# Kernel optimization log

Measured on AMD Instinct MI355X. Metric: run time of the kernel, lower is better.

The kernel has to match this reference:

```python
import jax, jax.numpy as jnp
import numpy as np

A_MAX = 7  # 2**A_bits - 1 with A_bits=3
W_HI = 7   # torch.randint(0, 2**W_bits - 1) -> values in [0, 6]


def _conv_valid(x, w):
    # x: [N,C,H,W] float32, w: [O,I,kh,kw] float32; stride 1, no padding
    return jax.lax.conv_general_dilated(
        x, w, window_strides=(1, 1), padding='VALID',
        dimension_numbers=('NCHW', 'OIHW', 'NCHW'))


def setup_inputs() -> dict:
    key = jax.random.key(0)
    k_x, k_w = jax.random.split(key)
    x = jax.random.randint(k_x, (16, 64, 112, 112), 0, 8, dtype=jnp.int32)
    # 3-bit weights of the original 7x7 conv, values 0..6
    W7 = jax.random.randint(k_w, (128, 64, 7, 7), 0, W_HI).astype(jnp.float32)
    w1 = W7[:, :, :, 0:3]
    w2 = W7[:, :, :, 2:5]
    w2 = w2.at[:, :, :, 0].set(0.0)
    w2 = w2.at[:, :, :, 2].set(0.0)
    w3 = W7[:, :, :, 4:7]
    return {"x": x, "w1": w1, "w2": w2, "w3": w3}


def reference(x, w1, w2, w3):
    # 3-bit activation quantization: clip int input to [0, 7]
    xc = jnp.clip(x, 0, A_MAX).astype(jnp.float32)
    out1 = _conv_valid(xc[:, :, :, :-2], w1)   # [N,O,H-6,W-4]
    out2 = _conv_valid(xc, w2)                 # [N,O,H-6,W-2]
    out3 = _conv_valid(xc[:, :, :, 2:], w3)    # [N,O,H-6,W-4]
    # combine slices -> equivalent to valid 7x7 conv: [N,O,H-6,W-6]
    return out1[:, :, :, :-2] + out2[:, :, :, 2:-2] + out3[:, :, :, 2:]
```

## Files before the change

kernel.cpp:

```cpp
#include <hip/hip_runtime.h>
#include <cstdint>

typedef __attribute__((ext_vector_type(4))) int i32x4;

#define XROWS  22
#define ROWB   2048
#define WSLICE 8192
#define WB_BYTES 409600
#define XT_BYTES ((size_t)16 * 112 * 128 * 64)
#define NTILES 1568
#define GRID_MAIN 1536

__device__ __forceinline__ void g2lds16(const void* g, void* l) {
  __builtin_amdgcn_global_load_lds(
      (const __attribute__((address_space(1))) unsigned int*)g,
      (__attribute__((address_space(3))) unsigned int*)l, 16, 0, 0);
}

__global__ void prep_w(const float* __restrict__ w1,
                       const float* __restrict__ w2,
                       const float* __restrict__ w3,
                       signed char* __restrict__ wb) {
  int t = blockIdx.x * 256 + threadIdx.x;
  int lo = t & 15;
  int co = (t >> 4) & 127;
  int g  = (t >> 11) & 3;
  int s  = t >> 13;
  if (s >= 49) return;
  int kh = s / 7, kw = s % 7;
  int ci = g * 16 + lo;
  int base = ((co * 64 + ci) * 7 + kh) * 3;
  float v;
  if (kw < 3)       v = w1[base + kw];
  else if (kw == 3) v = w2[base + 1];
  else              v = w3[base + kw - 4];
  wb[t] = (signed char)(int)v;
}

__global__ void prep_xw(const int* __restrict__ x,
                        const float* __restrict__ w1,
                        const float* __restrict__ w2,
                        const float* __restrict__ w3,
                        signed char* __restrict__ xt,
                        signed char* __restrict__ wb) {
  __shared__ unsigned char T[64 * 68];
  const int tid = threadIdx.x;
  const int wt = blockIdx.x * 64, h = blockIdx.y, n = blockIdx.z;
  const int fid = (blockIdx.z * 112 + blockIdx.y) * 2 + blockIdx.x;

  if (fid < 1568) {
    int t = fid * 256 + tid;
    int lo = t & 15;
    int co = (t >> 4) & 127;
    int g  = (t >> 11) & 3;
    int s  = t >> 13;
    int kh = s / 7, kw = s % 7;
    int ci = g * 16 + lo;
    int base = ((co * 64 + ci) * 7 + kh) * 3;
    float v;
    if (kw < 3)       v = w1[base + kw];
    else if (kw == 3) v = w2[base + 1];
    else              v = w3[base + kw - 4];
    wb[t] = (signed char)(int)v;
  }

  {
    const int wr = tid & 63;
    const int cb = (tid >> 6) * 16;
    int ws = wt + wr; ws = ws < 112 ? ws : 111;
    const int* xp = x + (((size_t)n * 64 + cb) * 112 + h) * 112 + ws;
    #pragma unroll
    for (int g4 = 0; g4 < 4; ++g4) {
      uint32_t v = 0;
      #pragma unroll
      for (int j = 0; j < 4; ++j) {
        int a = xp[(g4 * 4 + j) * 12544];
        a = a < 0 ? 0 : (a > 7 ? 7 : a);
        v |= (uint32_t)a << (8 * j);
      }
      *(uint32_t*)&T[wr * 68 + cb + g4 * 4] = v;
    }
  }
  __syncthreads();
  {
    const int wo = tid >> 2, q = tid & 3;
    const int key = ((wt + wo) >> 1) & 3;
    const int sg = (q ^ key) << 4;
    int4 v;
    v.x = *(const int*)&T[wo * 68 + sg + 0];
    v.y = *(const int*)&T[wo * 68 + sg + 4];
    v.z = *(const int*)&T[wo * 68 + sg + 8];
    v.w = *(const int*)&T[wo * 68 + sg + 12];
    *(int4*)&xt[(((size_t)n * 112 + h) * 128 + wt + wo) * 64 + q * 16] = v;
  }
}

#define MFMA(acc, a, b) acc = __builtin_amdgcn_mfma_i32_16x16x64_i8(a, b, acc, 0, 0, 0)

__global__ __launch_bounds__(256, 3)
void conv7s(const signed char* __restrict__ xt,
            const signed char* __restrict__ wb,
            float* __restrict__ out) {
  __shared__ __align__(16) unsigned char Xs[XROWS * ROWB];

  const int tid  = threadIdx.x;
  const int lane = tid & 63;
  const int wid  = tid >> 6;
  const int lrow = lane & 15;
  const int lkg  = lane >> 4;

  const int L  = blockIdx.x;
  const int Lp = (L & 7) * 192 + (L >> 3);
  const int npass = (L < 32) ? 2 : 1;

  for (int pass = 0; pass < npass; ++pass) {
    const int t = (pass == 0) ? Lp : (GRID_MAIN + L);
    const int coh = t & 1;
    const int r2  = t >> 1;
    const int bx  = r2 % 7;
    const int t7  = r2 / 7;
    const int by  = t7 % 7;
    const int n   = t7 / 7;
    const int ho_base = by * 16;
    const int wo_base = bx * 16;

    const signed char* aB = wb + lkg * 2048 + (coh * 64 + wid * 16 + lrow) * 16;

    i32x4 Aa = *(const i32x4*)aB;
    i32x4 Ab;

    if (pass) __syncthreads();

    for (int r = wid; r < XROWS; r += 4) {
      int h = ho_base + r; h = h < 112 ? h : 111;
      const signed char* src = xt + (((size_t)n * 112 + h) * 128 + wo_base) * 64;
      g2lds16(src + lane * 16, &Xs[r * ROWB]);
      g2lds16(src + 1024 + lane * 16, &Xs[r * ROWB + 1024]);
    }
    asm volatile("s_waitcnt vmcnt(0)" ::: "memory");
    __syncthreads();

    i32x4 acc[16];
    #pragma unroll
    for (int j = 0; j < 16; ++j) acc[j] = (i32x4){0, 0, 0, 0};

    for (int kw = 0; kw < 7; ++kw) {
      const int w_l  = lrow + kw;
      const int bcol = w_l * 64 + ((lkg ^ ((w_l >> 1) & 3)) << 4);
      i32x4 B[16];
      #pragma unroll
      for (int b = 0; b < 16; ++b)
        B[b] = *(const i32x4*)&Xs[b * ROWB + bcol];

      #pragma unroll
      for (int kh = 0; kh < 7; ++kh) {
        const signed char* apn =
            aB + (size_t)(kh < 6 ? (kh + 1) * 7 + kw : (kw < 6 ? kw + 1 : 0)) * WSLICE;
        __builtin_amdgcn_s_setprio(1);
        if ((kh & 1) == 0) {
          Ab = *(const i32x4*)apn;
          #pragma unroll
          for (int j = 0; j < 16; ++j)
            MFMA(acc[j], Aa, B[(kh + j) & 15]);
        } else {
          Aa = *(const i32x4*)apn;
          #pragma unroll
          for (int j = 0; j < 16; ++j)
            MFMA(acc[j], Ab, B[(kh + j) & 15]);
        }
        __builtin_amdgcn_s_setprio(0);
        if (kh < 6)
          B[kh] = *(const i32x4*)&Xs[(kh + 16) * ROWB + bcol];
      }
      Aa = Ab;
    }

    const int wo = wo_base + lrow;
    if (wo < 106) {
      const int co = coh * 64 + wid * 16 + lkg * 4;
      #pragma unroll
      for (int j = 0; j < 16; ++j) {
        const int ho = ho_base + j;
        if (ho < 106) {
          float* op = out + (((size_t)n * 128 + co) * 106 + ho) * 106 + wo;
          #pragma unroll
          for (int jj = 0; jj < 4; ++jj)
            op[(size_t)jj * 11236] = (float)acc[j][jj];
        }
      }
    }
  }
}

__global__ __launch_bounds__(256, 3)
void conv7f(const int* __restrict__ x,
            const signed char* __restrict__ wb, float* __restrict__ out) {
  __shared__ __align__(16) unsigned char Xs[XROWS * ROWB];

  const int tid  = threadIdx.x;
  const int lane = tid & 63;
  const int wid  = tid >> 6;
  const int lrow = lane & 15;
  const int lkg  = lane >> 4;

  const int L  = blockIdx.x;
  const int Lp = (L & 7) * 196 + (L >> 3);
  const int coh = Lp & 1;
  const int r2  = Lp >> 1;
  const int bx  = r2 % 7;
  const int t7  = r2 / 7;
  const int by  = t7 % 7;
  const int n   = t7 / 7;
  const int ho_base = by * 16;
  const int wo_base = bx * 16;

  const signed char* aB = wb + lkg * 2048 + coh * 1024 + lrow * 16;
  i32x4 A[4];
  #pragma unroll
  for (int m = 0; m < 4; ++m) A[m] = *(const i32x4*)(aB + m * 256);

  {
    const int w_a  = tid & 15,       cg_a  = tid >> 4;
    const int w_b2 = 16 + (tid & 7), cg_b2 = tid >> 3;
    const bool doB = (tid < 128) && ((tid & 7) < 6);
    const int keyA = ((w_a >> 1) & 3) << 2;
    const int keyB = ((w_b2 >> 1) & 3) << 2;
    for (int r = 0; r < XROWS; ++r) {
      int h = ho_base + r; h = h < 112 ? h : 111;
      const int* xr = x + (size_t)n * 64 * 12544 + h * 112;
      {
        int wc = wo_base + w_a; wc = wc < 112 ? wc : 111;
        uint32_t v = 0;
        #pragma unroll
        for (int j = 0; j < 4; ++j) {
          int a = xr[(cg_a * 4 + j) * 12544 + wc];
          a = a < 0 ? 0 : (a > 7 ? 7 : a);
          v |= (uint32_t)a << (8 * j);
        }
        *(uint32_t*)&Xs[r * ROWB + w_a * 64 + ((cg_a ^ keyA) << 2)] = v;
      }
      if (doB) {
        int wc = wo_base + w_b2; wc = wc < 112 ? wc : 111;
        uint32_t v = 0;
        #pragma unroll
        for (int j = 0; j < 4; ++j) {
          int a = xr[(cg_b2 * 4 + j) * 12544 + wc];
          a = a < 0 ? 0 : (a > 7 ? 7 : a);
          v |= (uint32_t)a << (8 * j);
        }
        *(uint32_t*)&Xs[r * ROWB + w_b2 * 64 + ((cg_b2 ^ keyB) << 2)] = v;
      }
    }
  }
  __syncthreads();

  i32x4 acc[4][4];
  #pragma unroll
  for (int m = 0; m < 4; ++m)
    #pragma unroll
    for (int b = 0; b < 4; ++b)
      acc[m][b] = (i32x4){0, 0, 0, 0};

  const int rowB = wid * 4;

  for (int kw = 0; kw < 7; ++kw) {
    const int w_l  = lrow + kw;
    const int bcol = w_l * 64 + ((lkg ^ ((w_l >> 1) & 3)) << 4);
    i32x4 B[8];
    #pragma unroll
    for (int b = 0; b < 4; ++b)
      B[b] = *(const i32x4*)&Xs[(rowB + b) * ROWB + bcol];
    #pragma unroll
    for (int kh = 0; kh < 7; ++kh) {
      if (kh < 6)
        B[(kh + 4) & 7] = *(const i32x4*)&Xs[(rowB + kh + 4) * ROWB + bcol];
      const signed char* apn = aB + (size_t)(kh < 6 ? (kh + 1) * 7 + kw : kw + 1) * WSLICE;
      #pragma unroll
      for (int m = 0; m < 4; ++m) {
        #pragma unroll
        for (int b = 0; b < 4; ++b)
          MFMA(acc[m][b], A[m], B[(kh + b) & 7]);
        A[m] = *(const i32x4*)(apn + m * 256);
      }
    }
  }

  const int wo = wo_base + lrow;
  if (wo < 106) {
    #pragma unroll
    for (int m = 0; m < 4; ++m) {
      const int co = coh * 64 + m * 16 + lkg * 4;
      #pragma unroll
      for (int b = 0; b < 4; ++b) {
        const int ho = ho_base + rowB + b;
        if (ho < 106) {
          float* op = out + (((size_t)n * 128 + co) * 106 + ho) * 106 + wo;
          #pragma unroll
          for (int j = 0; j < 4; ++j)
            op[(size_t)j * 11236] = (float)acc[m][b][j];
        }
      }
    }
  }
}

extern "C" void kernel_launch(void* const* d_in, const int* in_sizes, int n_in,
                              void* d_out, int out_size, void* d_ws, size_t ws_size,
                              hipStream_t stream) {
  const int*   x  = (const int*)d_in[0];
  const float* w1 = (const float*)d_in[1];
  const float* w2 = (const float*)d_in[2];
  const float* w3 = (const float*)d_in[3];
  float* outp = (float*)d_out;
  signed char* wbp = (signed char*)d_ws;
  signed char* xtp = wbp + WB_BYTES;

  if (ws_size >= WB_BYTES + XT_BYTES) {
    prep_xw<<<dim3(2, 112, 16), dim3(256), 0, stream>>>(x, w1, w2, w3, xtp, wbp);
    conv7s<<<dim3(GRID_MAIN), dim3(256), 0, stream>>>(xtp, wbp, outp);
  } else {
    prep_w<<<dim3(1568), dim3(256), 0, stream>>>(w1, w2, w3, wbp);
    conv7f<<<dim3(1568), dim3(256), 0, stream>>>(x, wbp, outp);
  }
}
```

Before: 70.95 us.

## Switch main conv kernel from 16x16x64 to 32x32x32 int8 MFMA tiles

Rewrites the main convolution kernel to use 32x32x32 int8 MFMA instructions instead of 16x16x64. Each wave now covers 32 output channels by two interleaved output rows, and K is split into two 32-channel halves. The weight prep layout is reordered to match the new K split. The goal is fewer MFMA issues and fewer LDS B-fragment loads per output element. The cost is a new register and accumulator layout, larger 16-wide accumulators, and a more scattered store pattern.

```diff
diff --git a/kernel.cpp b/kernel.cpp
--- a/kernel.cpp
+++ b/kernel.cpp
@@ -2,13 +2,12 @@
 #include <cstdint>
 
 typedef __attribute__((ext_vector_type(4))) int i32x4;
+typedef __attribute__((ext_vector_type(16))) int i32x16;
 
 #define XROWS  22
 #define ROWB   2048
-#define WSLICE 8192
 #define WB_BYTES 409600
 #define XT_BYTES ((size_t)16 * 112 * 128 * 64)
-#define NTILES 1568
 #define GRID_MAIN 1536
 
 __device__ __forceinline__ void g2lds16(const void* g, void* l) {
@@ -50,12 +49,13 @@
 
   if (fid < 1568) {
     int t = fid * 256 + tid;
-    int lo = t & 15;
+    int b  = t & 15;
     int co = (t >> 4) & 127;
-    int g  = (t >> 11) & 3;
+    int hk = (t >> 11) & 1;
+    int k2 = (t >> 12) & 1;
     int s  = t >> 13;
     int kh = s / 7, kw = s % 7;
-    int ci = g * 16 + lo;
+    int ci = k2 * 32 + hk * 16 + b;
     int base = ((co * 64 + ci) * 7 + kh) * 3;
     float v;
     if (kw < 3)       v = w1[base + kw];
@@ -95,10 +95,11 @@
   }
 }
 
-#define MFMA(acc, a, b) acc = __builtin_amdgcn_mfma_i32_16x16x64_i8(a, b, acc, 0, 0, 0)
+#define MFMA16(acc, a, b) acc = __builtin_amdgcn_mfma_i32_16x16x64_i8(a, b, acc, 0, 0, 0)
+#define MFMA32(acc, a, b) acc = __builtin_amdgcn_mfma_i32_32x32x32_i8(a, b, acc, 0, 0, 0)
 
 __global__ __launch_bounds__(256, 3)
-void conv7s(const signed char* __restrict__ xt,
+void conv32(const signed char* __restrict__ xt,
             const signed char* __restrict__ wb,
             float* __restrict__ out) {
   __shared__ __align__(16) unsigned char Xs[XROWS * ROWB];
@@ -106,8 +107,12 @@
   const int tid  = threadIdx.x;
   const int lane = tid & 63;
   const int wid  = tid >> 6;
-  const int lrow = lane & 15;
-  const int lkg  = lane >> 4;
+  const int l15  = lane & 15;
+  const int l4   = (lane >> 4) & 1;
+  const int l5   = lane >> 5;
+  const int cohalf = wid >> 1;
+  const int sph    = wid & 1;
+  const int spbase = sph * 8;
 
   const int L  = blockIdx.x;
   const int Lp = (L & 7) * 192 + (L >> 3);
@@ -124,10 +129,8 @@
     const int ho_base = by * 16;
     const int wo_base = bx * 16;
 
-    const signed char* aB = wb + lkg * 2048 + (coh * 64 + wid * 16 + lrow) * 16;
-
-    i32x4 Aa = *(const i32x4*)aB;
-    i32x4 Ab;
+    const signed char* aB =
+        wb + l5 * 2048 + (coh * 64 + cohalf * 32 + (lane & 31)) * 16;
 
     if (pass) __syncthreads();
 
@@ -140,52 +143,71 @@
     asm volatile("s_waitcnt vmcnt(0)" ::: "memory");
     __syncthreads();
 
-    i32x4 acc[16];
-    #pragma unroll
-    for (int j = 0; j < 16; ++j) acc[j] = (i32x4){0, 0, 0, 0};
+    i32x16 acc[4];
+    #pragma unroll
+    for (int tt = 0; tt < 4; ++tt)
+      acc[tt] = (i32x16){0,0,0,0, 0,0,0,0, 0,0,0,0, 0,0,0,0};
+
+    i32x4 Aa = *(const i32x4*)aB;
+    i32x4 Ab;
 
     for (int kw = 0; kw < 7; ++kw) {
-      const int w_l  = lrow + kw;
-      const int bcol = w_l * 64 + ((lkg ^ ((w_l >> 1) & 3)) << 4);
-      i32x4 B[16];
-      #pragma unroll
-      for (int b = 0; b < 16; ++b)
-        B[b] = *(const i32x4*)&Xs[b * ROWB + bcol];
-
-      #pragma unroll
-      for (int kh = 0; kh < 7; ++kh) {
-        const signed char* apn =
-            aB + (size_t)(kh < 6 ? (kh + 1) * 7 + kw : (kw < 6 ? kw + 1 : 0)) * WSLICE;
-        __builtin_amdgcn_s_setprio(1);
-        if ((kh & 1) == 0) {
-          Ab = *(const i32x4*)apn;
+      const int w_l = l15 + kw;
+      const int key = (w_l >> 1) & 3;
+      const int rbase = (spbase + l4) * ROWB + w_l * 64;
+      const int cb0 = rbase + (((0 + l5) ^ key) << 4);
+      const int cb1 = rbase + (((2 + l5) ^ key) << 4);
+      #pragma unroll
+      for (int k2 = 0; k2 < 2; ++k2) {
+        const int cb = k2 ? cb1 : cb0;
+        i32x4 Be[4], Bo[4];
+        #pragma unroll
+        for (int p = 0; p < 4; ++p) {
+          Be[p] = *(const i32x4*)&Xs[cb + (2 * p) * ROWB];
+          Bo[p] = *(const i32x4*)&Xs[cb + (2 * p + 1) * ROWB];
+        }
+        #pragma unroll
+        for (int kh = 0; kh < 7; ++kh) {
+          const int nkh = (kh < 6) ? kh + 1 : 0;
+          const int nk2 = (kh < 6) ? k2 : (k2 ^ 1);
+          const int nkw = (kh < 6) ? kw : (k2 == 0 ? kw : (kw < 6 ? kw + 1 : 0));
+          const signed char* apn = aB + (size_t)((nkh * 7 + nkw) * 2 + nk2) * 4096;
+          __builtin_amdgcn_s_setprio(1);
+          if ((kh & 1) == 0) {
+            Ab = *(const i32x4*)apn;
+            #pragma unroll
+            for (int tt = 0; tt < 4; ++tt)
+              MFMA32(acc[tt], Aa, Be[(tt + (kh >> 1)) & 3]);
+          } else {
+            Aa = *(const i32x4*)apn;
+            #pragma unroll
+            for (int tt = 0; tt < 4; ++tt)
+              MFMA32(acc[tt], Ab, Bo[(tt + (kh >> 1)) & 3]);
+          }
+          __builtin_amdgcn_s_setprio(0);
+          if (kh == 0)      Be[0] = *(const i32x4*)&Xs[cb +  8 * ROWB];
+          else if (kh == 1) Bo[0] = *(const i32x4*)&Xs[cb +  9 * ROWB];
+          else if (kh == 2) Be[1] = *(const i32x4*)&Xs[cb + 10 * ROWB];
+          else if (kh == 3) Bo[1] = *(const i32x4*)&Xs[cb + 11 * ROWB];
+          else if (kh == 4) Be[2] = *(const i32x4*)&Xs[cb + 12 * ROWB];
+        }
+        Aa = Ab;
+      }
+    }
+
+    const int wo = wo_base + l15;
+    if (wo < 106) {
+      #pragma unroll
+      for (int tt = 0; tt < 4; ++tt) {
+        const int ho = ho_base + spbase + 2 * tt + l4;
+        if (ho < 106) {
+          float* op = out +
+              (((size_t)n * 128 + coh * 64 + cohalf * 32) * 106 + ho) * 106 + wo;
           #pragma unroll
-          for (int j = 0; j < 16; ++j)
-            MFMA(acc[j], Aa, B[(kh + j) & 15]);
-        } else {
-          Aa = *(const i32x4*)apn;
-          #pragma unroll
-          for (int j = 0; j < 16; ++j)
-            MFMA(acc[j], Ab, B[(kh + j) & 15]);
-        }
-        __builtin_amdgcn_s_setprio(0);
-        if (kh < 6)
-          B[kh] = *(const i32x4*)&Xs[(kh + 16) * ROWB + bcol];
-      }
-      Aa = Ab;
-    }
-
-    const int wo = wo_base + lrow;
-    if (wo < 106) {
-      const int co = coh * 64 + wid * 16 + lkg * 4;
-      #pragma unroll
-      for (int j = 0; j < 16; ++j) {
-        const int ho = ho_base + j;
-        if (ho < 106) {
-          float* op = out + (((size_t)n * 128 + co) * 106 + ho) * 106 + wo;
-          #pragma unroll
-          for (int jj = 0; jj < 4; ++jj)
-            op[(size_t)jj * 11236] = (float)acc[j][jj];
+          for (int j = 0; j < 16; ++j) {
+            const int r = (j & 3) + 8 * (j >> 2) + 4 * l5;
+            op[(size_t)r * 11236] = (float)acc[tt][j];
+          }
         }
       }
     }
@@ -274,12 +296,12 @@
     for (int kh = 0; kh < 7; ++kh) {
       if (kh < 6)
         B[(kh + 4) & 7] = *(const i32x4*)&Xs[(rowB + kh + 4) * ROWB + bcol];
-      const signed char* apn = aB + (size_t)(kh < 6 ? (kh + 1) * 7 + kw : kw + 1) * WSLICE;
+      const signed char* apn = aB + (size_t)(kh < 6 ? (kh + 1) * 7 + kw : kw + 1) * 8192;
       #pragma unroll
       for (int m = 0; m < 4; ++m) {
         #pragma unroll
         for (int b = 0; b < 4; ++b)
-          MFMA(acc[m][b], A[m], B[(kh + b) & 7]);
+          MFMA16(acc[m][b], A[m], B[(kh + b) & 7]);
         A[m] = *(const i32x4*)(apn + m * 256);
       }
     }
@@ -317,7 +339,7 @@
 
   if (ws_size >= WB_BYTES + XT_BYTES) {
     prep_xw<<<dim3(2, 112, 16), dim3(256), 0, stream>>>(x, w1, w2, w3, xtp, wbp);
-    conv7s<<<dim3(GRID_MAIN), dim3(256), 0, stream>>>(xtp, wbp, outp);
+    conv32<<<dim3(GRID_MAIN), dim3(256), 0, stream>>>(xtp, wbp, outp);
   } else {
     prep_w<<<dim3(1568), dim3(256), 0, stream>>>(w1, w2, w3, wbp);
     conv7f<<<dim3(1568), dim3(256), 0, stream>>>(x, wbp, outp);
```

After: 108.3 us. 1.53x slower.
